# Kernel optimization log

Measured on AMD Instinct MI355X. Metric: run time of the kernel, lower is better.

## Reference

```python
import jax, jax.numpy as jnp
import numpy as np

N = 100000   # num nodes
D = 256      # latent_dim
B = 4096     # batch nodes
K = 32       # max padded degree per view
NREL = 9     # relation types 0..8
TEMP = 0.07

VIEW1_RELS = np.array([0, 7, 8])
VIEW2_RELS = np.array([1, 2, 3, 4, 5, 6])


def setup_inputs() -> dict:
    key = jax.random.key(0)
    ks = jax.random.split(key, 16)
    inv_sqrt_d = 1.0 / np.sqrt(D)
    node_features = jax.random.normal(ks[0], (N, D), dtype=jnp.float32)
    rel_emb = jax.random.normal(ks[1], (NREL, D), dtype=jnp.float32) * 0.1
    nb_ids1 = jax.random.randint(ks[2], (B, K), 0, N)
    nb_ids2 = jax.random.randint(ks[3], (B, K), 0, N)
    rel_ids1 = jnp.asarray(VIEW1_RELS)[jax.random.randint(ks[4], (B, K), 0, len(VIEW1_RELS))]
    rel_ids2 = jnp.asarray(VIEW2_RELS)[jax.random.randint(ks[5], (B, K), 0, len(VIEW2_RELS))]
    mask1 = jax.random.randint(ks[6], (B, K), 0, 2).astype(bool)
    mask2 = jax.random.randint(ks[7], (B, K), 0, 2).astype(bool)
    batch_node_ids = jax.random.randint(ks[8], (B,), 0, N)
    W1a = jax.random.normal(ks[9], (D, D), dtype=jnp.float32) * inv_sqrt_d
    b1a = jnp.zeros((D,), dtype=jnp.float32)
    W1b = jax.random.normal(ks[10], (D, D // 2), dtype=jnp.float32) * inv_sqrt_d
    b1b = jnp.zeros((D // 2,), dtype=jnp.float32)
    W2a = jax.random.normal(ks[11], (D, D), dtype=jnp.float32) * inv_sqrt_d
    b2a = jnp.zeros((D,), dtype=jnp.float32)
    W2b = jax.random.normal(ks[12], (D, D // 2), dtype=jnp.float32) * inv_sqrt_d
    b2b = jnp.zeros((D // 2,), dtype=jnp.float32)
    return dict(node_features=node_features, rel_emb=rel_emb,
                nb_ids1=nb_ids1, rel_ids1=rel_ids1, mask1=mask1,
                nb_ids2=nb_ids2, rel_ids2=rel_ids2, mask2=mask2,
                batch_node_ids=batch_node_ids,
                W1a=W1a, b1a=b1a, W1b=W1b, b1b=b1b,
                W2a=W2a, b2a=b2a, W2b=W2b, b2b=b2b)


def _aggregate(nf, rel_emb, nb_ids, rel_ids, mask, self_ids):
    # [B,K,D] messages = neighbor feature + relation embedding
    msg = nf[nb_ids] + rel_emb[rel_ids]
    m = mask[..., None].astype(nf.dtype)
    cnt = mask.sum(axis=-1).astype(nf.dtype)            # [B]
    mean = (msg * m).sum(axis=1) / jnp.maximum(cnt, 1.0)[:, None]
    # nodes with no neighbors fall back to their own feature
    return jnp.where((cnt > 0)[:, None], mean, nf[self_ids])


def _proj(x, Wa, ba, Wb, bb):
    h = jax.nn.relu(x @ Wa + ba)
    return h @ Wb + bb


def _infonce(z1, z2, temperature):
    z1 = z1 / jnp.linalg.norm(z1, axis=-1, keepdims=True)
    z2 = z2 / jnp.linalg.norm(z2, axis=-1, keepdims=True)
    sim = (z1 @ z2.T) / temperature                      # [B,B]
    lsm12 = jax.nn.log_softmax(sim, axis=-1)
    lsm21 = jax.nn.log_softmax(sim.T, axis=-1)
    diag = jnp.arange(sim.shape[0])
    loss_12 = -lsm12[diag, diag].mean()
    loss_21 = -lsm21[diag, diag].mean()
    return (loss_12 + loss_21) / 2


def reference(node_features, rel_emb, nb_ids1, rel_ids1, mask1,
              nb_ids2, rel_ids2, mask2, batch_node_ids,
              W1a, b1a, W1b, b1b, W2a, b2a, W2b, b2b):
    v1 = _aggregate(node_features, rel_emb, nb_ids1, rel_ids1, mask1, batch_node_ids)
    v2 = _aggregate(node_features, rel_emb, nb_ids2, rel_ids2, mask2, batch_node_ids)
    z1 = _proj(v1, W1a, b1a, W1b, b1b)
    z2 = _proj(v2, W2a, b2a, W2b, b2b)
    return _infonce(z1, z2, TEMP)
```

## Files before the change

kernel.cpp:

```cpp
#include <hip/hip_runtime.h>
#include <hip/hip_bf16.h>
#include <math.h>

#define NN 100000
#define DD 256
#define BB 4096
#define KK 32
#define ZD 128
#define INVTEMP (1.0f/0.07f)
#define HS 264

typedef unsigned short u16;
typedef __attribute__((ext_vector_type(8))) short short8;
typedef __attribute__((ext_vector_type(4))) float floatx4;

__device__ inline u16 f2bf(float f) {
  __hip_bfloat16 h = __float2bfloat16(f);
  return *reinterpret_cast<u16*>(&h);
}

__global__ void convw_all(const float* __restrict__ W1a, const float* __restrict__ W2a,
                          const float* __restrict__ W1b, const float* __restrict__ W2b,
                          u16* __restrict__ W1at, u16* __restrict__ W2at,
                          u16* __restrict__ W1bt, u16* __restrict__ W2bt) {
  int idx = blockIdx.x * 256 + threadIdx.x;
  const float* W; u16* Wt; int N, off;
  if (idx < 65536)       { W = W1a; Wt = W1at; N = 256; off = idx; }
  else if (idx < 131072) { W = W2a; Wt = W2at; N = 256; off = idx - 65536; }
  else if (idx < 163840) { W = W1b; Wt = W1bt; N = 128; off = idx - 131072; }
  else                   { W = W2b; Wt = W2bt; N = 128; off = idx - 163840; }
  int n = off >> 8, k = off & 255;
  Wt[off] = f2bf(W[k * N + n]);
}

__global__ void aggregate_kernel(const float* __restrict__ nf,
                                 const float* __restrict__ rel,
                                 const int* __restrict__ nb1, const int* __restrict__ rl1, const int* __restrict__ mk1,
                                 const int* __restrict__ nb2, const int* __restrict__ rl2, const int* __restrict__ mk2,
                                 const int* __restrict__ self_ids,
                                 u16* __restrict__ v1, u16* __restrict__ v2) {
  int b = blockIdx.x;
  const int *nb, *rl, *mk;
  u16* out;
  if (blockIdx.y == 0) { nb = nb1; rl = rl1; mk = mk1; out = v1; }
  else                 { nb = nb2; rl = rl2; mk = mk2; out = v2; }
  int tid = threadIdx.x;
  int g = tid >> 6, c = tid & 63;

  float ax = 0.f, ay = 0.f, az = 0.f, aw = 0.f;
  int cnt = 0;
#pragma unroll
  for (int kk = 0; kk < 8; ++kk) {
    int k = kk * 4 + g;
    if (mk[b * KK + k]) {
      int nid = nb[b * KK + k];
      int rid = rl[b * KK + k];
      float4 m = *(const float4*)(nf + (size_t)nid * DD + c * 4);
      float4 r = *(const float4*)(rel + (size_t)rid * DD + c * 4);
      ax += m.x + r.x; ay += m.y + r.y; az += m.z + r.z; aw += m.w + r.w;
      cnt++;
    }
  }
  __shared__ float sbuf[4][64][4];
  __shared__ int scnt[4];
  sbuf[g][c][0] = ax; sbuf[g][c][1] = ay; sbuf[g][c][2] = az; sbuf[g][c][3] = aw;
  if (c == 0) scnt[g] = cnt;
  __syncthreads();
  if (g == 0) {
    float sx = sbuf[0][c][0] + sbuf[1][c][0] + sbuf[2][c][0] + sbuf[3][c][0];
    float sy = sbuf[0][c][1] + sbuf[1][c][1] + sbuf[2][c][1] + sbuf[3][c][1];
    float sz = sbuf[0][c][2] + sbuf[1][c][2] + sbuf[2][c][2] + sbuf[3][c][2];
    float sw = sbuf[0][c][3] + sbuf[1][c][3] + sbuf[2][c][3] + sbuf[3][c][3];
    int tot = scnt[0] + scnt[1] + scnt[2] + scnt[3];
    float rx, ry, rz, rw;
    if (tot > 0) {
      float inv = 1.0f / (float)tot;
      rx = sx * inv; ry = sy * inv; rz = sz * inv; rw = sw * inv;
    } else {
      float4 s = *(const float4*)(nf + (size_t)self_ids[b] * DD + c * 4);
      rx = s.x; ry = s.y; rz = s.z; rw = s.w;
    }
    union { u16 us[4]; uint2 u2; } pk;
    pk.us[0] = f2bf(rx); pk.us[1] = f2bf(ry); pk.us[2] = f2bf(rz); pk.us[3] = f2bf(rw);
    *(uint2*)(out + (size_t)b * DD + c * 4) = pk.u2;
  }
}

__global__ void __launch_bounds__(256, 1)
proj_fused(const u16* __restrict__ v1, const u16* __restrict__ v2,
           const u16* __restrict__ W1at, const u16* __restrict__ W2at,
           const float* __restrict__ b1a, const float* __restrict__ b2a,
           const u16* __restrict__ W1bt, const u16* __restrict__ W2bt,
           const float* __restrict__ b1b, const float* __restrict__ b2b,
           float* __restrict__ z1f, float* __restrict__ z2f) {
  const u16 *v, *Wat, *Wbt;
  const float *ba, *bb;
  float* zf;
  if (blockIdx.y == 0) { v = v1; Wat = W1at; ba = b1a; Wbt = W1bt; bb = b1b; zf = z1f; }
  else                 { v = v2; Wat = W2at; ba = b2a; Wbt = W2bt; bb = b2b; zf = z2f; }
  __shared__ u16 hs[128 * HS];
  int tid = threadIdx.x;
  int lane = tid & 63, wid = tid >> 6;
  int m16 = lane & 15, q = lane >> 4;
  int rh = wid >> 1, ch = wid & 1;
  int M0 = blockIdx.x * 128;
  int rowl = rh * 64;

  for (int nt = 0; nt < 2; ++nt) {
    int colb = nt * 128 + ch * 64;
    floatx4 acc[4][4] = {};
    for (int k0 = 0; k0 < DD; k0 += 32) {
      short8 a[4], b[4];
#pragma unroll
      for (int i = 0; i < 4; i++)
        a[i] = *(const short8*)(v + (size_t)(M0 + rowl + i * 16 + m16) * DD + k0 + q * 8);
#pragma unroll
      for (int j = 0; j < 4; j++)
        b[j] = *(const short8*)(Wat + (size_t)(colb + j * 16 + m16) * DD + k0 + q * 8);
#pragma unroll
      for (int i = 0; i < 4; i++)
#pragma unroll
        for (int j = 0; j < 4; j++)
          acc[i][j] = __builtin_amdgcn_mfma_f32_16x16x32_bf16(a[i], b[j], acc[i][j], 0, 0, 0);
    }
#pragma unroll
    for (int i = 0; i < 4; i++)
#pragma unroll
      for (int j = 0; j < 4; j++) {
        int col = colb + j * 16 + m16;
        float bv = ba[col];
#pragma unroll
        for (int r = 0; r < 4; r++) {
          int row = rowl + i * 16 + q * 4 + r;
          hs[row * HS + col] = f2bf(fmaxf(acc[i][j][r] + bv, 0.f));
        }
      }
  }
  __syncthreads();

  {
    int colb = ch * 64;
    floatx4 acc[4][4] = {};
    for (int k0 = 0; k0 < DD; k0 += 32) {
      short8 a[4], b[4];
#pragma unroll
      for (int i = 0; i < 4; i++)
        a[i] = *(const short8*)(hs + (rowl + i * 16 + m16) * HS + k0 + q * 8);
#pragma unroll
      for (int j = 0; j < 4; j++)
        b[j] = *(const short8*)(Wbt + (size_t)(colb + j * 16 + m16) * DD + k0 + q * 8);
#pragma unroll
      for (int i = 0; i < 4; i++)
#pragma unroll
        for (int j = 0; j < 4; j++)
          acc[i][j] = __builtin_amdgcn_mfma_f32_16x16x32_bf16(a[i], b[j], acc[i][j], 0, 0, 0);
    }
#pragma unroll
    for (int i = 0; i < 4; i++)
#pragma unroll
      for (int j = 0; j < 4; j++) {
        int col = colb + j * 16 + m16;
        float bv = bb[col];
#pragma unroll
        for (int r = 0; r < 4; r++) {
          int row = M0 + rowl + i * 16 + q * 4 + r;
          zf[(size_t)row * ZD + col] = acc[i][j][r] + bv;
        }
      }
  }
}

__global__ void normalize_diag(const float* __restrict__ z1f, const float* __restrict__ z2f,
                               u16* __restrict__ z1, u16* __restrict__ z2,
                               float* __restrict__ diag,
                               float* __restrict__ rowsum, float* __restrict__ colsum) {
  int i = blockIdx.x, t = threadIdx.x;
  if (t == 0) { rowsum[i] = 0.f; colsum[i] = 0.f; }
  float2 a = *(const float2*)(z1f + (size_t)i * ZD + t * 2);
  float2 b = *(const float2*)(z2f + (size_t)i * ZD + t * 2);
  float s1 = a.x * a.x + a.y * a.y;
  float s2 = b.x * b.x + b.y * b.y;
#pragma unroll
  for (int off = 1; off < 64; off <<= 1) {
    s1 += __shfl_xor(s1, off);
    s2 += __shfl_xor(s2, off);
  }
  float n1 = rsqrtf(s1), n2 = rsqrtf(s2);
  float ax = a.x * n1, ay = a.y * n1;
  float bx = b.x * n2, by = b.y * n2;
  union { u16 us[2]; unsigned u; } p1, p2;
  p1.us[0] = f2bf(ax); p1.us[1] = f2bf(ay);
  p2.us[0] = f2bf(bx); p2.us[1] = f2bf(by);
  *(unsigned*)(z1 + (size_t)i * ZD + t * 2) = p1.u;
  *(unsigned*)(z2 + (size_t)i * ZD + t * 2) = p2.u;
  float d = ax * bx + ay * by;
#pragma unroll
  for (int off = 1; off < 64; off <<= 1) d += __shfl_xor(d, off);
  if (t == 0) diag[i] = d * INVTEMP;
}

__global__ void __launch_bounds__(256, 2)
sim_kernel(const u16* __restrict__ z1, const u16* __restrict__ z2,
           float* __restrict__ rowsum, float* __restrict__ colsum) {
  int tid = threadIdx.x;
  int lane = tid & 63, wid = tid >> 6;
  int m16 = lane & 15, q = lane >> 4;
  int rowbase = blockIdx.x * 128 + (wid >> 1) * 64;
  int colbase = blockIdx.y * 128 + (wid & 1) * 64;
  floatx4 acc[4][4] = {};
  for (int k0 = 0; k0 < ZD; k0 += 32) {
    short8 a[4], b[4];
#pragma unroll
    for (int i = 0; i < 4; i++)
      a[i] = *(const short8*)(z1 + (size_t)(rowbase + i * 16 + m16) * ZD + k0 + q * 8);
#pragma unroll
    for (int j = 0; j < 4; j++)
      b[j] = *(const short8*)(z2 + (size_t)(colbase + j * 16 + m16) * ZD + k0 + q * 8);
#pragma unroll
    for (int i = 0; i < 4; i++)
#pragma unroll
      for (int j = 0; j < 4; j++)
        acc[i][j] = __builtin_amdgcn_mfma_f32_16x16x32_bf16(a[i], b[j], acc[i][j], 0, 0, 0);
  }
  float rowacc[4][4] = {};
  float colacc[4] = {};
#pragma unroll
  for (int i = 0; i < 4; i++)
#pragma unroll
    for (int j = 0; j < 4; j++)
#pragma unroll
      for (int r = 0; r < 4; r++) {
        float e = __expf(acc[i][j][r] * INVTEMP);
        rowacc[i][r] += e;
        colacc[j] += e;
      }
#pragma unroll
  for (int off = 1; off <= 8; off <<= 1)
#pragma unroll
    for (int i = 0; i < 4; i++)
#pragma unroll
      for (int r = 0; r < 4; r++) rowacc[i][r] += __shfl_xor(rowacc[i][r], off);
  if (m16 == 0) {
#pragma unroll
    for (int i = 0; i < 4; i++)
#pragma unroll
      for (int r = 0; r < 4; r++)
        atomicAdd(&rowsum[rowbase + i * 16 + q * 4 + r], rowacc[i][r]);
  }
#pragma unroll
  for (int off = 16; off <= 32; off <<= 1)
#pragma unroll
    for (int j = 0; j < 4; j++) colacc[j] += __shfl_xor(colacc[j], off);
  if (q == 0) {
#pragma unroll
    for (int j = 0; j < 4; j++)
      atomicAdd(&colsum[colbase + j * 16 + m16], colacc[j]);
  }
}

__global__ void loss_kernel(const float* __restrict__ rowsum, const float* __restrict__ colsum,
                            const float* __restrict__ diag, float* __restrict__ out) {
  int tid = threadIdx.x;
  float acc = 0.f;
  for (int i = tid; i < BB; i += 256)
    acc += 0.5f * (logf(rowsum[i]) + logf(colsum[i])) - diag[i];
#pragma unroll
  for (int off = 1; off < 64; off <<= 1) acc += __shfl_xor(acc, off);
  __shared__ float sbuf[4];
  if ((tid & 63) == 0) sbuf[tid >> 6] = acc;
  __syncthreads();
  if (tid == 0) out[0] = (sbuf[0] + sbuf[1] + sbuf[2] + sbuf[3]) * (1.0f / BB);
}

extern "C" void kernel_launch(void* const* d_in, const int* in_sizes, int n_in,
                              void* d_out, int out_size, void* d_ws, size_t ws_size,
                              hipStream_t stream) {
  const float* nf  = (const float*)d_in[0];
  const float* rel = (const float*)d_in[1];
  const int* nb1 = (const int*)d_in[2];
  const int* rl1 = (const int*)d_in[3];
  const int* mk1 = (const int*)d_in[4];
  const int* nb2 = (const int*)d_in[5];
  const int* rl2 = (const int*)d_in[6];
  const int* mk2 = (const int*)d_in[7];
  const int* self_ids = (const int*)d_in[8];
  const float* W1a = (const float*)d_in[9];
  const float* b1a = (const float*)d_in[10];
  const float* W1b = (const float*)d_in[11];
  const float* b1b = (const float*)d_in[12];
  const float* W2a = (const float*)d_in[13];
  const float* b2a = (const float*)d_in[14];
  const float* W2b = (const float*)d_in[15];
  const float* b2b = (const float*)d_in[16];

  char* ws = (char*)d_ws;
  u16* v1   = (u16*)ws;                 ws += (size_t)BB * DD * 2;
  u16* v2   = (u16*)ws;                 ws += (size_t)BB * DD * 2;
  float* z1f = (float*)ws;              ws += (size_t)BB * ZD * 4;
  float* z2f = (float*)ws;              ws += (size_t)BB * ZD * 4;
  u16* z1   = (u16*)ws;                 ws += (size_t)BB * ZD * 2;
  u16* z2   = (u16*)ws;                 ws += (size_t)BB * ZD * 2;
  u16* W1at = (u16*)ws;                 ws += (size_t)DD * DD * 2;
  u16* W2at = (u16*)ws;                 ws += (size_t)DD * DD * 2;
  u16* W1bt = (u16*)ws;                 ws += (size_t)ZD * DD * 2;
  u16* W2bt = (u16*)ws;                 ws += (size_t)ZD * DD * 2;
  float* rowsum = (float*)ws;           ws += (size_t)BB * 4;
  float* colsum = (float*)ws;           ws += (size_t)BB * 4;
  float* diag   = (float*)ws;           ws += (size_t)BB * 4;

  convw_all<<<768, 256, 0, stream>>>(W1a, W2a, W1b, W2b, W1at, W2at, W1bt, W2bt);
  aggregate_kernel<<<dim3(BB, 2), 256, 0, stream>>>(nf, rel, nb1, rl1, mk1,
                                                    nb2, rl2, mk2, self_ids, v1, v2);
  proj_fused<<<dim3(BB / 128, 2), 256, 0, stream>>>(v1, v2, W1at, W2at, b1a, b2a,
                                                    W1bt, W2bt, b1b, b2b, z1f, z2f);
  normalize_diag<<<BB, 64, 0, stream>>>(z1f, z2f, z1, z2, diag, rowsum, colsum);
  sim_kernel<<<dim3(BB / 128, BB / 128), 256, 0, stream>>>(z1, z2, rowsum, colsum);
  loss_kernel<<<1, 256, 0, stream>>>(rowsum, colsum, diag, (float*)d_out);
}
```

Baseline: 255.3 us.

## Fuse pipeline into three kernels: merged prep, in-GEMM normalize, last-block loss

```diff
diff --git a/kernel.cpp b/kernel.cpp
--- a/kernel.cpp
+++ b/kernel.cpp
@@ -9,6 +9,7 @@
 #define ZD 128
 #define INVTEMP (1.0f/0.07f)
 #define HS 264
+#define SIMBLOCKS ((BB/128)*(BB/128))
 
 typedef unsigned short u16;
 typedef __attribute__((ext_vector_type(8))) short short8;
@@ -19,32 +20,40 @@
   return *reinterpret_cast<u16*>(&h);
 }
 
-__global__ void convw_all(const float* __restrict__ W1a, const float* __restrict__ W2a,
-                          const float* __restrict__ W1b, const float* __restrict__ W2b,
-                          u16* __restrict__ W1at, u16* __restrict__ W2at,
-                          u16* __restrict__ W1bt, u16* __restrict__ W2bt) {
-  int idx = blockIdx.x * 256 + threadIdx.x;
-  const float* W; u16* Wt; int N, off;
-  if (idx < 65536)       { W = W1a; Wt = W1at; N = 256; off = idx; }
-  else if (idx < 131072) { W = W2a; Wt = W2at; N = 256; off = idx - 65536; }
-  else if (idx < 163840) { W = W1b; Wt = W1bt; N = 128; off = idx - 131072; }
-  else                   { W = W2b; Wt = W2bt; N = 128; off = idx - 163840; }
-  int n = off >> 8, k = off & 255;
-  Wt[off] = f2bf(W[k * N + n]);
-}
-
-__global__ void aggregate_kernel(const float* __restrict__ nf,
-                                 const float* __restrict__ rel,
-                                 const int* __restrict__ nb1, const int* __restrict__ rl1, const int* __restrict__ mk1,
-                                 const int* __restrict__ nb2, const int* __restrict__ rl2, const int* __restrict__ mk2,
-                                 const int* __restrict__ self_ids,
-                                 u16* __restrict__ v1, u16* __restrict__ v2) {
-  int b = blockIdx.x;
+__global__ void prep_kernel(const float* __restrict__ nf,
+                            const float* __restrict__ rel,
+                            const int* __restrict__ nb1, const int* __restrict__ rl1, const int* __restrict__ mk1,
+                            const int* __restrict__ nb2, const int* __restrict__ rl2, const int* __restrict__ mk2,
+                            const int* __restrict__ self_ids,
+                            u16* __restrict__ v1, u16* __restrict__ v2,
+                            const float* __restrict__ W1a, const float* __restrict__ W2a,
+                            const float* __restrict__ W1b, const float* __restrict__ W2b,
+                            u16* __restrict__ W1at, u16* __restrict__ W2at,
+                            u16* __restrict__ W1bt, u16* __restrict__ W2bt,
+                            float* __restrict__ rowsum, float* __restrict__ colsum,
+                            unsigned* __restrict__ done) {
+  int blk = blockIdx.x;
+  int tid = threadIdx.x;
+  if (blk >= 2 * BB) {
+    int cb = blk - 2 * BB;
+    int idx = cb * 256 + tid;
+    const float* W; u16* Wt; int N, off;
+    if (idx < 65536)       { W = W1a; Wt = W1at; N = 256; off = idx; }
+    else if (idx < 131072) { W = W2a; Wt = W2at; N = 256; off = idx - 65536; }
+    else if (idx < 163840) { W = W1b; Wt = W1bt; N = 128; off = idx - 131072; }
+    else                   { W = W2b; Wt = W2bt; N = 128; off = idx - 163840; }
+    int n = off >> 8, k = off & 255;
+    Wt[off] = f2bf(W[k * N + n]);
+    if (cb < 16)            rowsum[cb * 256 + tid] = 0.f;
+    else if (cb < 32)       colsum[(cb - 16) * 256 + tid] = 0.f;
+    if (cb == 32 && tid == 0) *done = 0u;
+    return;
+  }
+  int b = blk >> 1;
   const int *nb, *rl, *mk;
   u16* out;
-  if (blockIdx.y == 0) { nb = nb1; rl = rl1; mk = mk1; out = v1; }
-  else                 { nb = nb2; rl = rl2; mk = mk2; out = v2; }
-  int tid = threadIdx.x;
+  if ((blk & 1) == 0) { nb = nb1; rl = rl1; mk = mk1; out = v1; }
+  else                { nb = nb2; rl = rl2; mk = mk2; out = v2; }
   int g = tid >> 6, c = tid & 63;
 
   float ax = 0.f, ay = 0.f, az = 0.f, aw = 0.f;
@@ -92,13 +101,14 @@
            const float* __restrict__ b1a, const float* __restrict__ b2a,
            const u16* __restrict__ W1bt, const u16* __restrict__ W2bt,
            const float* __restrict__ b1b, const float* __restrict__ b2b,
-           float* __restrict__ z1f, float* __restrict__ z2f) {
+           u16* __restrict__ z1, u16* __restrict__ z2) {
   const u16 *v, *Wat, *Wbt;
   const float *ba, *bb;
-  float* zf;
-  if (blockIdx.y == 0) { v = v1; Wat = W1at; ba = b1a; Wbt = W1bt; bb = b1b; zf = z1f; }
-  else                 { v = v2; Wat = W2at; ba = b2a; Wbt = W2bt; bb = b2b; zf = z2f; }
+  u16* z;
+  if (blockIdx.y == 0) { v = v1; Wat = W1at; ba = b1a; Wbt = W1bt; bb = b1b; z = z1; }
+  else                 { v = v2; Wat = W2at; ba = b2a; Wbt = W2bt; bb = b2b; z = z2; }
   __shared__ u16 hs[128 * HS];
+  __shared__ float ns[128][2];
   int tid = threadIdx.x;
   int lane = tid & 63, wid = tid >> 6;
   int m16 = lane & 15, q = lane >> 4;
@@ -138,70 +148,69 @@
   }
   __syncthreads();
 
-  {
-    int colb = ch * 64;
-    floatx4 acc[4][4] = {};
-    for (int k0 = 0; k0 < DD; k0 += 32) {
-      short8 a[4], b[4];
-#pragma unroll
-      for (int i = 0; i < 4; i++)
-        a[i] = *(const short8*)(hs + (rowl + i * 16 + m16) * HS + k0 + q * 8);
+  int colb = ch * 64;
+  floatx4 acc[4][4] = {};
+  for (int k0 = 0; k0 < DD; k0 += 32) {
+    short8 a[4], b[4];
+#pragma unroll
+    for (int i = 0; i < 4; i++)
+      a[i] = *(const short8*)(hs + (rowl + i * 16 + m16) * HS + k0 + q * 8);
+#pragma unroll
+    for (int j = 0; j < 4; j++)
+      b[j] = *(const short8*)(Wbt + (size_t)(colb + j * 16 + m16) * DD + k0 + q * 8);
+#pragma unroll
+    for (int i = 0; i < 4; i++)
 #pragma unroll
       for (int j = 0; j < 4; j++)
-        b[j] = *(const short8*)(Wbt + (size_t)(colb + j * 16 + m16) * DD + k0 + q * 8);
-#pragma unroll
-      for (int i = 0; i < 4; i++)
-#pragma unroll
-        for (int j = 0; j < 4; j++)
-          acc[i][j] = __builtin_amdgcn_mfma_f32_16x16x32_bf16(a[i], b[j], acc[i][j], 0, 0, 0);
-    }
-#pragma unroll
-    for (int i = 0; i < 4; i++)
-#pragma unroll
-      for (int j = 0; j < 4; j++) {
-        int col = colb + j * 16 + m16;
-        float bv = bb[col];
-#pragma unroll
-        for (int r = 0; r < 4; r++) {
-          int row = M0 + rowl + i * 16 + q * 4 + r;
-          zf[(size_t)row * ZD + col] = acc[i][j][r] + bv;
-        }
+        acc[i][j] = __builtin_amdgcn_mfma_f32_16x16x32_bf16(a[i], b[j], acc[i][j], 0, 0, 0);
+  }
+  float ss[4][4];
+#pragma unroll
+  for (int i = 0; i < 4; i++)
+#pragma unroll
+    for (int r = 0; r < 4; r++) ss[i][r] = 0.f;
+#pragma unroll
+  for (int j = 0; j < 4; j++) {
+    float bv = bb[colb + j * 16 + m16];
+#pragma unroll
+    for (int i = 0; i < 4; i++)
+#pragma unroll
+      for (int r = 0; r < 4; r++) {
+        float zv = acc[i][j][r] + bv;
+        acc[i][j][r] = zv;
+        ss[i][r] += zv * zv;
       }
   }
-}
-
-__global__ void normalize_diag(const float* __restrict__ z1f, const float* __restrict__ z2f,
-                               u16* __restrict__ z1, u16* __restrict__ z2,
-                               float* __restrict__ diag,
-                               float* __restrict__ rowsum, float* __restrict__ colsum) {
-  int i = blockIdx.x, t = threadIdx.x;
-  if (t == 0) { rowsum[i] = 0.f; colsum[i] = 0.f; }
-  float2 a = *(const float2*)(z1f + (size_t)i * ZD + t * 2);
-  float2 b = *(const float2*)(z2f + (size_t)i * ZD + t * 2);
-  float s1 = a.x * a.x + a.y * a.y;
-  float s2 = b.x * b.x + b.y * b.y;
-#pragma unroll
-  for (int off = 1; off < 64; off <<= 1) {
-    s1 += __shfl_xor(s1, off);
-    s2 += __shfl_xor(s2, off);
-  }
-  float n1 = rsqrtf(s1), n2 = rsqrtf(s2);
-  float ax = a.x * n1, ay = a.y * n1;
-  float bx = b.x * n2, by = b.y * n2;
-  union { u16 us[2]; unsigned u; } p1, p2;
-  p1.us[0] = f2bf(ax); p1.us[1] = f2bf(ay);
-  p2.us[0] = f2bf(bx); p2.us[1] = f2bf(by);
-  *(unsigned*)(z1 + (size_t)i * ZD + t * 2) = p1.u;
-  *(unsigned*)(z2 + (size_t)i * ZD + t * 2) = p2.u;
-  float d = ax * bx + ay * by;
-#pragma unroll
-  for (int off = 1; off < 64; off <<= 1) d += __shfl_xor(d, off);
-  if (t == 0) diag[i] = d * INVTEMP;
+#pragma unroll
+  for (int off = 1; off <= 8; off <<= 1)
+#pragma unroll
+    for (int i = 0; i < 4; i++)
+#pragma unroll
+      for (int r = 0; r < 4; r++) ss[i][r] += __shfl_xor(ss[i][r], off);
+  if (m16 == 0) {
+#pragma unroll
+    for (int i = 0; i < 4; i++)
+#pragma unroll
+      for (int r = 0; r < 4; r++) ns[rowl + i * 16 + q * 4 + r][ch] = ss[i][r];
+  }
+  __syncthreads();
+#pragma unroll
+  for (int i = 0; i < 4; i++)
+#pragma unroll
+    for (int r = 0; r < 4; r++) {
+      int row = rowl + i * 16 + q * 4 + r;
+      float rn = rsqrtf(ns[row][0] + ns[row][1]);
+#pragma unroll
+      for (int j = 0; j < 4; j++)
+        z[(size_t)(M0 + row) * ZD + colb + j * 16 + m16] = f2bf(acc[i][j][r] * rn);
+    }
 }
 
 __global__ void __launch_bounds__(256, 2)
 sim_kernel(const u16* __restrict__ z1, const u16* __restrict__ z2,
-           float* __restrict__ rowsum, float* __restrict__ colsum) {
+           float* __restrict__ rowsum, float* __restrict__ colsum,
+           float* __restrict__ diag, unsigned* __restrict__ done,
+           float* __restrict__ out) {
   int tid = threadIdx.x;
   int lane = tid & 63, wid = tid >> 6;
   int m16 = lane & 15, q = lane >> 4;
@@ -222,6 +231,14 @@
       for (int j = 0; j < 4; j++)
         acc[i][j] = __builtin_amdgcn_mfma_f32_16x16x32_bf16(a[i], b[j], acc[i][j], 0, 0, 0);
   }
+  if (rowbase == colbase) {
+#pragma unroll
+    for (int i = 0; i < 4; i++)
+#pragma unroll
+      for (int r = 0; r < 4; r++)
+        if (m16 == q * 4 + r)
+          diag[rowbase + i * 16 + m16] = acc[i][i][r] * INVTEMP;
+  }
   float rowacc[4][4] = {};
   float colacc[4] = {};
 #pragma unroll
@@ -256,20 +273,30 @@
     for (int j = 0; j < 4; j++)
       atomicAdd(&colsum[colbase + j * 16 + m16], colacc[j]);
   }
-}
-
-__global__ void loss_kernel(const float* __restrict__ rowsum, const float* __restrict__ colsum,
-                            const float* __restrict__ diag, float* __restrict__ out) {
-  int tid = threadIdx.x;
-  float acc = 0.f;
-  for (int i = tid; i < BB; i += 256)
-    acc += 0.5f * (logf(rowsum[i]) + logf(colsum[i])) - diag[i];
-#pragma unroll
-  for (int off = 1; off < 64; off <<= 1) acc += __shfl_xor(acc, off);
-  __shared__ float sbuf[4];
-  if ((tid & 63) == 0) sbuf[tid >> 6] = acc;
+
+  __shared__ unsigned lastflag;
+  __threadfence();
+  if (tid == 0) {
+    unsigned old = atomicAdd(done, 1u);
+    lastflag = (old == SIMBLOCKS - 1) ? 1u : 0u;
+  }
   __syncthreads();
-  if (tid == 0) out[0] = (sbuf[0] + sbuf[1] + sbuf[2] + sbuf[3]) * (1.0f / BB);
+  if (lastflag) {
+    __threadfence();
+    float acc2 = 0.f;
+    for (int i = tid; i < BB; i += 256) {
+      float rs = atomicAdd(&rowsum[i], 0.f);
+      float cs = atomicAdd(&colsum[i], 0.f);
+      float dg = atomicAdd(&diag[i], 0.f);
+      acc2 += 0.5f * (__logf(rs) + __logf(cs)) - dg;
+    }
+#pragma unroll
+    for (int off = 1; off < 64; off <<= 1) acc2 += __shfl_xor(acc2, off);
+    __shared__ float sred[4];
+    if ((tid & 63) == 0) sred[tid >> 6] = acc2;
+    __syncthreads();
+    if (tid == 0) out[0] = (sred[0] + sred[1] + sred[2] + sred[3]) * (1.0f / BB);
+  }
 }
 
 extern "C" void kernel_launch(void* const* d_in, const int* in_sizes, int n_in,
@@ -296,8 +323,6 @@
   char* ws = (char*)d_ws;
   u16* v1   = (u16*)ws;                 ws += (size_t)BB * DD * 2;
   u16* v2   = (u16*)ws;                 ws += (size_t)BB * DD * 2;
-  float* z1f = (float*)ws;              ws += (size_t)BB * ZD * 4;
-  float* z2f = (float*)ws;              ws += (size_t)BB * ZD * 4;
   u16* z1   = (u16*)ws;                 ws += (size_t)BB * ZD * 2;
   u16* z2   = (u16*)ws;                 ws += (size_t)BB * ZD * 2;
   u16* W1at = (u16*)ws;                 ws += (size_t)DD * DD * 2;
@@ -307,13 +332,15 @@
   float* rowsum = (float*)ws;           ws += (size_t)BB * 4;
   float* colsum = (float*)ws;           ws += (size_t)BB * 4;
   float* diag   = (float*)ws;           ws += (size_t)BB * 4;
-
-  convw_all<<<768, 256, 0, stream>>>(W1a, W2a, W1b, W2b, W1at, W2at, W1bt, W2bt);
-  aggregate_kernel<<<dim3(BB, 2), 256, 0, stream>>>(nf, rel, nb1, rl1, mk1,
-                                                    nb2, rl2, mk2, self_ids, v1, v2);
+  unsigned* done = (unsigned*)ws;       ws += 64;
+
+  prep_kernel<<<2 * BB + 768, 256, 0, stream>>>(nf, rel, nb1, rl1, mk1, nb2, rl2, mk2,
+                                                self_ids, v1, v2,
+                                                W1a, W2a, W1b, W2b,
+                                                W1at, W2at, W1bt, W2bt,
+                                                rowsum, colsum, done);
   proj_fused<<<dim3(BB / 128, 2), 256, 0, stream>>>(v1, v2, W1at, W2at, b1a, b2a,
-                                                    W1bt, W2bt, b1b, b2b, z1f, z2f);
-  normalize_diag<<<BB, 64, 0, stream>>>(z1f, z2f, z1, z2, diag, rowsum, colsum);
-  sim_kernel<<<dim3(BB / 128, BB / 128), 256, 0, stream>>>(z1, z2, rowsum, colsum);
-  loss_kernel<<<1, 256, 0, stream>>>(rowsum, colsum, diag, (float*)d_out);
-}
+                                                    W1bt, W2bt, b1b, b2b, z1, z2);
+  sim_kernel<<<dim3(BB / 128, BB / 128), 256, 0, stream>>>(z1, z2, rowsum, colsum,
+                                                           diag, done, (float*)d_out);
+}
```

After: 312.7 us. +22.5%, slower.
